# Kernel tuning notes

Hardware: AMD Instinct MI355X
Metric: run time of the kernel (lower is better)

## Reference

```python
import jax, jax.numpy as jnp
import numpy as np
from jax import lax

P = 4
PSIZE = P * P
ITERS = 3
EPS = 1e-8
LAMBDA = 1e-3  # inverse-temperature used by the EM routing sigmoid (yl-1993 style)
LN2PI_HALF = 0.5 * float(np.log(2.0 * np.pi))


def extract_patches(x, K, stride, pad):
    """x: (b,h,w,c) -> (b,oh,ow,K*K,c) sliding-window patches."""
    if pad:
        x = jnp.pad(x, ((0, 0), (pad, pad), (pad, pad), (0, 0)))
    b, h, w, c = x.shape
    oh = (h - K) // stride + 1
    ow = (w - K) // stride + 1
    slices = []
    for ki in range(K):
        for kj in range(K):
            slices.append(x[:, ki:ki + stride * (oh - 1) + 1:stride,
                             kj:kj + stride * (ow - 1) + 1:stride, :])
    return jnp.stack(slices, axis=3)  # (b,oh,ow,K*K,c)


def em_routing(v, a_in, beta_u, beta_a, iters=ITERS):
    """EM routing (Hinton et al. 2018).
    v: (n, Bin, Cout, PSIZE) votes, a_in: (n, Bin, 1) input activations.
    Returns mu: (n, Cout, PSIZE), a_out: (n, Cout).
    """
    n, Bin, Cout, psize = v.shape
    r = jnp.full((n, Bin, Cout), 1.0 / Cout, dtype=v.dtype)
    mu = None
    a_out = None
    for it in range(iters):
        # ---- M step ----
        r_w = r * a_in                                    # (n,Bin,Cout)
        r_sum = r_w.sum(axis=1, keepdims=True)            # (n,1,Cout)
        coeff = (r_w / (r_sum + EPS))[..., None]          # (n,Bin,Cout,1)
        mu = jnp.sum(coeff * v, axis=1, keepdims=True)    # (n,1,Cout,psize)
        sigma_sq = jnp.sum(coeff * (v - mu) ** 2, axis=1, keepdims=True) + EPS
        cost_h = (beta_u[None, None, :, None] + 0.5 * jnp.log(sigma_sq)) * r_sum[..., None]
        a_out = jax.nn.sigmoid(LAMBDA * (beta_a[None, None, :] - cost_h.sum(axis=3)))  # (n,1,Cout)
        # ---- E step ----
        if it < iters - 1:
            ln_p = -(v - mu) ** 2 / (2.0 * sigma_sq) - 0.5 * jnp.log(sigma_sq) - LN2PI_HALF
            ln_ap = ln_p.sum(axis=3) + jnp.log(EPS + a_out)  # (n,Bin,Cout)
            r = jax.nn.softmax(ln_ap, axis=2)
    return mu[:, 0], a_out[:, 0]


def depthwise_caps(pose, a, W, bu, ba, K, stride):
    """DepthWiseConvCaps: each capsule type routes its own KxK spatial patch to one
    output capsule of the same type. W: (K*K, B, P, P)."""
    b = pose.shape[0]
    Bc = a.shape[-1]
    pad = K // 2
    pp = extract_patches(pose, K, stride, pad)  # (b,oh,ow,KK,B*PSIZE)
    ap = extract_patches(a, K, stride, pad)     # (b,oh,ow,KK,B)
    oh, ow = pp.shape[1], pp.shape[2]
    pm = pp.reshape(b, oh, ow, K * K, Bc, P, P)
    v = jnp.einsum('bhwkcij,kcjl->bhwkcil', pm, W)            # (b,oh,ow,KK,B,P,P)
    v = v.transpose(0, 1, 2, 4, 3, 5, 6).reshape(b * oh * ow * Bc, K * K, 1, PSIZE)
    a_in = ap.transpose(0, 1, 2, 4, 3).reshape(b * oh * ow * Bc, K * K, 1)
    mu, a_out = em_routing(v, a_in, bu, ba)
    return mu.reshape(b, oh, ow, Bc * PSIZE), a_out.reshape(b, oh, ow, Bc)


def conv_caps_1x1(pose, a, W, bu, ba):
    """ConvCaps with K=1, stride=1: per-position routing Bin -> Cout. W: (Bin,Cout,P,P)."""
    b, h, w, _ = pose.shape
    Bc, Cc = W.shape[0], W.shape[1]
    pm = pose.reshape(b * h * w, Bc, P, P)
    v = jnp.einsum('nbij,bcjl->nbcil', pm, W).reshape(b * h * w, Bc, Cc, PSIZE)
    a_in = a.reshape(b * h * w, Bc)[..., None]
    mu, a_out = em_routing(v, a_in, bu, ba)
    return mu.reshape(b, h, w, Cc * PSIZE), a_out.reshape(b, h, w, Cc)


def class_caps(pose, a, W, bu, ba):
    """Class ConvCaps: w_shared across positions + coordinate addition. W: (D,E,P,P)."""
    b, h, w, _ = pose.shape
    D, E = W.shape[0], W.shape[1]
    pm = pose.reshape(b, h, w, D, P, P)
    v = jnp.einsum('bhwdij,dejl->bhwdeil', pm, W).reshape(b, h, w, D, E, PSIZE)
    # coordinate addition on the first two vote components
    coord = jnp.zeros((h, w, PSIZE), v.dtype)
    coord = coord.at[:, :, 0].add(jnp.arange(h, dtype=v.dtype)[:, None] / h)
    coord = coord.at[:, :, 1].add(jnp.arange(w, dtype=v.dtype)[None, :] / w)
    v = v + coord[None, :, :, None, None, :]
    v = v.reshape(b, h * w * D, E, PSIZE)
    a_in = a.reshape(b, h * w * D, 1)
    mu, a_out = em_routing(v, a_in, bu, ba)
    return mu, a_out  # (b,E,PSIZE), (b,E)


def _forward(x, conv1_w, conv1_b, prim_pose_w, prim_pose_b, prim_a_w, prim_a_b,
             dw1_w, dw1_bu, dw1_ba, cc1_w, cc1_bu, cc1_ba,
             dw2_w, dw2_bu, dw2_ba, cc2_w, cc2_bu, cc2_ba,
             cls_w, cls_bu, cls_ba):
    # conv stem: k5 s2 valid
    y = lax.conv_general_dilated(x, conv1_w, (2, 2), 'VALID',
                                 dimension_numbers=('NHWC', 'HWIO', 'NHWC'))
    y = jax.nn.relu(y + conv1_b)
    # primary caps: 1x1 convs for pose and activation
    pose = jnp.einsum('bhwc,cd->bhwd', y, prim_pose_w) + prim_pose_b   # (b,h,w,B*PSIZE)
    a = jax.nn.sigmoid(jnp.einsum('bhwc,cd->bhwd', y, prim_a_w) + prim_a_b)  # (b,h,w,B)
    pose, a = depthwise_caps(pose, a, dw1_w, dw1_bu, dw1_ba, K=7, stride=2)
    pose, a = conv_caps_1x1(pose, a, cc1_w, cc1_bu, cc1_ba)
    pose, a = depthwise_caps(pose, a, dw2_w, dw2_bu, dw2_ba, K=5, stride=2)
    pose, a = conv_caps_1x1(pose, a, cc2_w, cc2_bu, cc2_ba)
    pose_cls, a_cls = class_caps(pose, a, cls_w, cls_bu, cls_ba)
    return a_cls  # (b, E)


def setup_inputs() -> dict:
    key = jax.random.key(0)
    ks = jax.random.split(key, 10)
    f32 = jnp.float32
    d = {}
    d['x'] = jax.random.normal(ks[0], (32, 64, 64, 1), f32)
    d['conv1_w'] = jax.random.normal(ks[1], (5, 5, 1, 64), f32) * 0.1
    d['conv1_b'] = jnp.zeros((64,), f32)
    d['prim_pose_w'] = jax.random.normal(ks[2], (64, 128), f32) * 0.1
    d['prim_pose_b'] = jnp.zeros((128,), f32)
    d['prim_a_w'] = jax.random.normal(ks[3], (64, 8), f32) * 0.1
    d['prim_a_b'] = jnp.zeros((8,), f32)
    d['dw1_w'] = jax.random.normal(ks[4], (49, 8, 4, 4), f32) * 0.25
    d['dw1_bu'] = jnp.zeros((1,), f32)
    d['dw1_ba'] = jnp.zeros((1,), f32)
    d['cc1_w'] = jax.random.normal(ks[5], (8, 16, 4, 4), f32) * 0.25
    d['cc1_bu'] = jnp.zeros((16,), f32)
    d['cc1_ba'] = jnp.zeros((16,), f32)
    d['dw2_w'] = jax.random.normal(ks[6], (25, 16, 4, 4), f32) * 0.25
    d['dw2_bu'] = jnp.zeros((1,), f32)
    d['dw2_ba'] = jnp.zeros((1,), f32)
    d['cc2_w'] = jax.random.normal(ks[7], (16, 16, 4, 4), f32) * 0.25
    d['cc2_bu'] = jnp.zeros((16,), f32)
    d['cc2_ba'] = jnp.zeros((16,), f32)
    d['cls_w'] = jax.random.normal(ks[8], (16, 10, 4, 4), f32) * 0.25
    d['cls_bu'] = jnp.zeros((10,), f32)
    d['cls_ba'] = jnp.zeros((10,), f32)
    return d


def reference(x, conv1_w, conv1_b, prim_pose_w, prim_pose_b, prim_a_w, prim_a_b,
              dw1_w, dw1_bu, dw1_ba, cc1_w, cc1_bu, cc1_ba,
              dw2_w, dw2_bu, dw2_ba, cc2_w, cc2_bu, cc2_ba,
              cls_w, cls_bu, cls_ba):
    return _forward(x, conv1_w, conv1_b, prim_pose_w, prim_pose_b, prim_a_w, prim_a_b,
                    dw1_w, dw1_bu, dw1_ba, cc1_w, cc1_bu, cc1_ba,
                    dw2_w, dw2_bu, dw2_ba, cc2_w, cc2_bu, cc2_ba,
                    cls_w, cls_bu, cls_ba)
```

## Files before the change

### kernel.cpp

```cpp
#include <hip/hip_runtime.h>
#include <hip/hip_bf16.h>

#define EPS 1e-8f
#define LAMBDA 1e-3f
#define LN2PI_HALF 0.9189385332046727f

__device__ __forceinline__ float sigmoidf(float x) { return 1.f / (1.f + __expf(-x)); }

__global__ __launch_bounds__(256) void stem_primary_kernel(
    const float* __restrict__ x, const float* __restrict__ w,
    const float* __restrict__ bias,
    const float* __restrict__ wp, const float* __restrict__ bp,
    const float* __restrict__ wa, const float* __restrict__ ba,
    float* __restrict__ pose, float* __restrict__ a) {
  __shared__ float wp_s[64][128];
  __shared__ float wc_s[25][64];
  __shared__ float wa_s[64][8];
  __shared__ float bias_s[64];
  __shared__ float bp_s[128];
  __shared__ float ba_s[8];
  __shared__ float xs[5][23];
  __shared__ float ys[10][64];

  int t = threadIdx.x;
  int jt = blockIdx.x % 3;
  int oi = (blockIdx.x / 3) % 30;
  int b  = blockIdx.x / 90;
  int oj0 = jt * 10;

  for (int q = t; q < 8192; q += 256) ((float*)wp_s)[q] = wp[q];
  for (int q = t; q < 1600; q += 256) ((float*)wc_s)[q] = w[q];
  for (int q = t; q < 512;  q += 256) ((float*)wa_s)[q] = wa[q];
  if (t < 64) bias_s[t] = bias[t];
  if (t < 128) bp_s[t] = bp[t];
  if (t < 8) ba_s[t] = ba[t];
  for (int q = t; q < 115; q += 256) {
    int ki = q / 23, kj = q % 23;
    xs[ki][kj] = x[(b * 64 + 2 * oi + ki) * 64 + 2 * oj0 + kj];
  }
  __syncthreads();

#pragma unroll
  for (int rep = 0; rep < 3; ++rep) {
    int q = rep * 256 + t;
    if (q < 640) {
      int pos = q >> 6, ch = q & 63;
      float s = bias_s[ch];
#pragma unroll
      for (int ki = 0; ki < 5; ++ki)
#pragma unroll
        for (int kj = 0; kj < 5; ++kj)
          s += xs[ki][2 * pos + kj] * wc_s[ki * 5 + kj][ch];
      ys[pos][ch] = fmaxf(s, 0.f);
    }
  }
  __syncthreads();

  int w_ = t >> 7, d = t & 127;
  float acc[5];
#pragma unroll
  for (int j = 0; j < 5; ++j) acc[j] = bp_s[d];
  for (int c = 0; c < 64; ++c) {
    float wv = wp_s[c][d];
#pragma unroll
    for (int j = 0; j < 5; ++j) acc[j] += ys[w_ + 2 * j][c] * wv;
  }
  size_t rowbase = (size_t)(b * 30 + oi) * 30 + oj0;
#pragma unroll
  for (int j = 0; j < 5; ++j)
    pose[(rowbase + w_ + 2 * j) * 128 + d] = acc[j];

  if (t < 80) {
    int pos = t >> 3, jj = t & 7;
    float s = ba_s[jj];
#pragma unroll 8
    for (int c = 0; c < 64; ++c) s += ys[pos][c] * wa_s[c][jj];
    a[(rowbase + pos) * 8 + jj] = sigmoidf(s);
  }
}

template <int K, int BC, int HIN, int WIN, int HOUT, int WOUT, int OIG, int NG>
__global__ __launch_bounds__(256) void dw_caps_kernel(
    const float* __restrict__ pose_in, const float* __restrict__ a_in,
    const float* __restrict__ Wt,
    const float* __restrict__ bu_p, const float* __restrict__ ba_p,
    float* __restrict__ pose_out, float* __restrict__ a_out) {
  constexpr int PAD = K / 2;
  constexpr int RA = (2 * (OIG - 1) + K < HIN) ? (2 * (OIG - 1) + K) : HIN;
  __shared__ float tp[RA * WIN * 20];
  __shared__ float ta[RA * WIN];
  __shared__ float wt[K * K * 16];

  int t = threadIdx.x;
  int g = (NG > 1) ? (blockIdx.x % NG) : 0;
  int c = (blockIdx.x / NG) % BC;
  int b = blockIdx.x / (NG * BC);
  int oi_lo = g * OIG;
  int rlo = max(0, 2 * oi_lo - PAD);
  int rhi = min(HIN, 2 * (oi_lo + OIG - 1) - PAD + K);
  int nrows = rhi - rlo;

  for (int q = t; q < K * K * 16; q += 256) {
    int tap = q >> 4, lj = q & 15, l = lj >> 2, j = lj & 3;
    wt[tap * 16 + lj] = Wt[((size_t)tap * BC + c) * 16 + j * 4 + l];
  }
  for (int q = t; q < nrows * WIN; q += 256) {
    int row = q / WIN, col = q % WIN;
    ta[q] = a_in[((size_t)((b * HIN + rlo + row) * WIN + col)) * BC + c];
  }
  for (int q = t; q < nrows * WIN * 4; q += 256) {
    int quad = q & 3, pc = q >> 2;
    int row = pc / WIN, col = pc % WIN;
    const float4 src = *(const float4*)(pose_in +
        (((size_t)((b * HIN + rlo + row) * WIN + col)) * BC + c) * 16 + quad * 4);
    *(float4*)(tp + (row * WIN + col) * 20 + quad * 4) = src;
  }
  __syncthreads();

  for (int s = t; s < OIG * WOUT * 16; s += 256) {
    int p = s & 15, pr = s >> 4;
    int oj = pr % WOUT;
    int oi = oi_lo + pr / WOUT;
    int ip = p >> 2, l = p & 3;
    int ih0 = 2 * oi - PAD, iw0 = 2 * oj - PAD;
    float rsum = 0.f, acc = 0.f, acc2 = 0.f;
#pragma unroll
    for (int ki = 0; ki < K; ++ki) {
      int ih = ih0 + ki;
      if (ih < 0 || ih >= HIN) continue;
      int rbase = (ih - rlo) * WIN;
#pragma unroll
      for (int kj = 0; kj < K; ++kj) {
        int iw = iw0 + kj;
        if (iw < 0 || iw >= WIN) continue;
        float ak = ta[rbase + iw];
        const float4 pm = *(const float4*)(tp + (rbase + iw) * 20 + ip * 4);
        const float4 wr = *(const float4*)(wt + (ki * K + kj) * 16 + l * 4);
        float v = pm.x * wr.x + pm.y * wr.y + pm.z * wr.z + pm.w * wr.w;
        rsum += ak;
        float av = ak * v;
        acc += av;
        acc2 += av * v;
      }
    }
    float inv = 1.f / (rsum + EPS);
    float mu = acc * inv;
    float S = rsum * inv;
    float sg = acc2 * inv - mu * mu * (2.f - S);
    sg = fmaxf(sg, 0.f) + EPS;
    float hl = 0.5f * __logf(sg);
    float ls = hl;
    ls += __shfl_xor(ls, 1, 64);
    ls += __shfl_xor(ls, 2, 64);
    ls += __shfl_xor(ls, 4, 64);
    ls += __shfl_xor(ls, 8, 64);

    size_t obase = ((size_t)(b * HOUT + oi) * WOUT + oj) * BC + c;
    pose_out[obase * 16 + p] = mu;
    if (p == 0) {
      float cost = rsum * (16.f * bu_p[0] + ls);
      a_out[obase] = sigmoidf(LAMBDA * (ba_p[0] - cost));
    }
  }
}

template <int BIN>
__global__ __launch_bounds__(256) void cc_em_kernel(
    const float* __restrict__ pose_in, const float* __restrict__ a_arr,
    const float* __restrict__ Wt,
    const float* __restrict__ bu_p, const float* __restrict__ ba_p,
    float* __restrict__ pose_out, float* __restrict__ a_out) {
  constexpr int COUT = 16;
  __shared__ float pm_s[BIN * 16];
  __shared__ float ain_s[BIN];
  __shared__ float v_s[BIN][COUT * 16];
  __shared__ float rw_s[BIN][COUT];
  __shared__ float mu_s[COUT * 16];
  __shared__ float sg_s[COUT * 16];
  __shared__ float hl_s[COUT * 16];
  __shared__ float rsum_s[COUT];
  __shared__ float aout_s[COUT];
  __shared__ float lnap_s[BIN][COUT];

  int n = blockIdx.x, t = threadIdx.x;
  int c = t >> 4, p = t & 15;
  if (t < BIN * 16) pm_s[t] = pose_in[(size_t)n * BIN * 16 + t];
  if (t < BIN) ain_s[t] = a_arr[(size_t)n * BIN + t];
  __syncthreads();

  int ip = p >> 2, l = p & 3;
#pragma unroll
  for (int b = 0; b < BIN; ++b) {
    const float* wr = Wt + (b * COUT + c) * 16 + l;
    const float* pm = &pm_s[b * 16 + ip * 4];
    v_s[b][t] = pm[0] * wr[0] + pm[1] * wr[4] + pm[2] * wr[8] + pm[3] * wr[12];
  }
  if (t < BIN * COUT) rw_s[t / COUT][t % COUT] = (1.f / COUT) * ain_s[t / COUT];
  __syncthreads();

  for (int it = 0; it < 3; ++it) {
    if (t < COUT) {
      float s = 0.f;
#pragma unroll
      for (int b = 0; b < BIN; ++b) s += rw_s[b][t];
      rsum_s[t] = s;
    }
    __syncthreads();
    {
      float s = 0.f;
#pragma unroll
      for (int b = 0; b < BIN; ++b) s += rw_s[b][c] * v_s[b][t];
      float mu = s / (rsum_s[c] + EPS);
      mu_s[t] = mu;
      float s2 = 0.f;
#pragma unroll
      for (int b = 0; b < BIN; ++b) { float d = v_s[b][t] - mu; s2 += rw_s[b][c] * d * d; }
      float sg = s2 / (rsum_s[c] + EPS) + EPS;
      sg_s[t] = sg;
      hl_s[t] = 0.5f * __logf(sg);
    }
    __syncthreads();
    if (t < COUT) {
      float lsum = 0.f;
#pragma unroll
      for (int pp = 0; pp < 16; ++pp) lsum += hl_s[t * 16 + pp];
      float cost = rsum_s[t] * (16.f * bu_p[t] + lsum);
      aout_s[t] = sigmoidf(LAMBDA * (ba_p[t] - cost));
    }
    __syncthreads();
    if (it < 2) {
      if (t < BIN * COUT) {
        int b = t / COUT, cc = t % COUT;
        float s = __logf(EPS + aout_s[cc]) - 16.f * LN2PI_HALF;
#pragma unroll
        for (int pp = 0; pp < 16; ++pp) {
          float d = v_s[b][cc * 16 + pp] - mu_s[cc * 16 + pp];
          s += -d * d / (2.f * sg_s[cc * 16 + pp]) - hl_s[cc * 16 + pp];
        }
        lnap_s[b][cc] = s;
      }
      __syncthreads();
      if (t < BIN * COUT) {
        int b = t / COUT, cc = t % COUT;
        float m = -1e30f;
#pragma unroll
        for (int q = 0; q < COUT; ++q) m = fmaxf(m, lnap_s[b][q]);
        float Z = 0.f;
#pragma unroll
        for (int q = 0; q < COUT; ++q) Z += __expf(lnap_s[b][q] - m);
        rw_s[b][cc] = (__expf(lnap_s[b][cc] - m) / Z) * ain_s[b];
      }
      __syncthreads();
    }
  }
  pose_out[(size_t)n * COUT * 16 + t] = mu_s[t];
  if (t < COUT) a_out[(size_t)n * COUT + t] = aout_s[t];
}

__global__ __launch_bounds__(256) void cls_m_kernel(
    const float* __restrict__ pose5, const float* __restrict__ a5,
    const float* __restrict__ X, const float* __restrict__ W,
    const float* __restrict__ bu_p, const float* __restrict__ ba_p,
    float* __restrict__ mu_g, float* __restrict__ inv2_g,
    float* __restrict__ base_g, float* __restrict__ out,
    int first, int last) {
  int blk = blockIdx.x;
  int c = blk % 10, b = blk / 10;
  int t = threadIdx.x;
  int lane = t & 63, wv = t >> 6;
  const float* pg = pose5 + (size_t)b * 16384;
  __shared__ float w_s[16][16];
  {
    int d = t & 15, jj = t >> 4;
    w_s[jj][d] = W[(d * 10 + c) * 16 + jj];
  }
  __syncthreads();
  const int d = t & 15;
  float wf[16];
#pragma unroll
  for (int jj = 0; jj < 16; ++jj) wf[jj] = w_s[jj][d];

  float sA = 0.f, sV[16], sV2[16];
#pragma unroll
  for (int p = 0; p < 16; ++p) { sV[p] = 0.f; sV2[p] = 0.f; }
#pragma unroll
  for (int rep = 0; rep < 4; ++rep) {
    int bi = rep * 256 + t;
    int pos = bi >> 4;
    float rw = first ? 0.1f * a5[(size_t)b * 1024 + bi]
                     : X[(size_t)blk * 1024 + bi];
    float ci = (float)(pos >> 3) * 0.125f;
    float cj = (float)(pos & 7) * 0.125f;
    const float* pp = pg + pos * 256 + d * 16;
    float pmr[16];
#pragma unroll
    for (int q = 0; q < 16; ++q) pmr[q] = pp[q];
    sA += rw;
#pragma unroll
    for (int p = 0; p < 16; ++p) {
      int ip = p >> 2, l = p & 3;
      float v = pmr[ip * 4 + 0] * wf[0 * 4 + l] + pmr[ip * 4 + 1] * wf[1 * 4 + l]
              + pmr[ip * 4 + 2] * wf[2 * 4 + l] + pmr[ip * 4 + 3] * wf[3 * 4 + l];
      if (p == 0) v += ci;
      else if (p == 1) v += cj;
      float rv = rw * v;
      sV[p] += rv;
      sV2[p] += rv * v;
    }
  }
#pragma unroll
  for (int off = 1; off < 64; off <<= 1) {
    sA += __shfl_xor(sA, off, 64);
#pragma unroll
    for (int p = 0; p < 16; ++p) {
      sV[p]  += __shfl_xor(sV[p],  off, 64);
      sV2[p] += __shfl_xor(sV2[p], off, 64);
    }
  }
  __shared__ float red[4][36];
  if (lane == 0) {
    red[wv][0] = sA;
#pragma unroll
    for (int p = 0; p < 16; ++p) { red[wv][1 + p] = sV[p]; red[wv][17 + p] = sV2[p]; }
  }
  __syncthreads();
  if (t < 16) {
    int p = t;
    float sAf  = red[0][0] + red[1][0] + red[2][0] + red[3][0];
    float sVf  = red[0][1+p] + red[1][1+p] + red[2][1+p] + red[3][1+p];
    float sV2f = red[0][17+p] + red[1][17+p] + red[2][17+p] + red[3][17+p];
    float inv = 1.f / (sAf + EPS);
    float S = sAf * inv;
    float mu = sVf * inv;
    float sg = sV2f * inv - mu * mu * (2.f - S) + EPS;
    sg = fmaxf(sg, EPS);
    mu_g[blk * 16 + p] = mu;
    inv2_g[blk * 16 + p] = 0.5f / sg;
    float hl = 0.5f * __logf(sg);
    float lsum = hl;
    lsum += __shfl_xor(lsum, 1, 64);
    lsum += __shfl_xor(lsum, 2, 64);
    lsum += __shfl_xor(lsum, 4, 64);
    lsum += __shfl_xor(lsum, 8, 64);
    if (p == 0) {
      float cost = sAf * (16.f * bu_p[c] + lsum);
      float ao = sigmoidf(LAMBDA * (ba_p[c] - cost));
      base_g[blk] = __logf(EPS + ao) - lsum - 16.f * LN2PI_HALF;
      if (last) out[blk] = ao;
    }
  }
}

__global__ __launch_bounds__(512) void cls_e_kernel(
    const float* __restrict__ pose5, const float* __restrict__ a5,
    const float* __restrict__ W,
    const float* __restrict__ mu_g, const float* __restrict__ inv2_g,
    const float* __restrict__ base_g, float* __restrict__ X) {
  int b = blockIdx.x >> 1;
  int t = threadIdx.x;
  int bi = ((blockIdx.x & 1) << 9) + t;
  const float* pg = pose5 + (size_t)b * 16384;
  __shared__ float w2[10][16][16];
  __shared__ float mu_s[160];
  __shared__ float inv2_s[160];
  __shared__ float base_s[10];
  for (int q = t; q < 2560; q += 512) {
    int dd = q & 15, jj = (q >> 4) & 15, c = q >> 8;
    w2[c][jj][dd] = W[(dd * 10 + c) * 16 + jj];
  }
  if (t < 160) { mu_s[t] = mu_g[b * 160 + t]; inv2_s[t] = inv2_g[b * 160 + t]; }
  if (t >= 160 && t < 170) base_s[t - 160] = base_g[b * 10 + (t - 160)];
  __syncthreads();

  int pos = bi >> 4, d2 = bi & 15;
  float ci = (float)(pos >> 3) * 0.125f;
  float cj = (float)(pos & 7) * 0.125f;
  const float* pp = pg + pos * 256 + d2 * 16;
  float pmr[16];
#pragma unroll
  for (int q = 0; q < 16; ++q) pmr[q] = pp[q];
  float lnap[10];
#pragma unroll
  for (int c = 0; c < 10; ++c) {
    float wf[16];
#pragma unroll
    for (int jj = 0; jj < 16; ++jj) wf[jj] = w2[c][jj][d2];
    float s = base_s[c];
#pragma unroll
    for (int p = 0; p < 16; ++p) {
      int ip = p >> 2, l = p & 3;
      float v = pmr[ip * 4 + 0] * wf[0 * 4 + l] + pmr[ip * 4 + 1] * wf[1 * 4 + l]
              + pmr[ip * 4 + 2] * wf[2 * 4 + l] + pmr[ip * 4 + 3] * wf[3 * 4 + l];
      if (p == 0) v += ci;
      else if (p == 1) v += cj;
      float dd = v - mu_s[c * 16 + p];
      s -= dd * dd * inv2_s[c * 16 + p];
    }
    lnap[c] = s;
  }
  float m = -1e30f;
#pragma unroll
  for (int c = 0; c < 10; ++c) m = fmaxf(m, lnap[c]);
  float Z = 0.f;
  float ex[10];
#pragma unroll
  for (int c = 0; c < 10; ++c) { ex[c] = __expf(lnap[c] - m); Z += ex[c]; }
  float invZ = a5[(size_t)b * 1024 + bi] / Z;
#pragma unroll
  for (int c = 0; c < 10; ++c) X[((size_t)(b * 10 + c)) * 1024 + bi] = ex[c] * invZ;
}

extern "C" void kernel_launch(void* const* d_in, const int* in_sizes, int n_in,
                              void* d_out, int out_size, void* d_ws, size_t ws_size,
                              hipStream_t stream) {
  const float* x       = (const float*)d_in[0];
  const float* conv1_w = (const float*)d_in[1];
  const float* conv1_b = (const float*)d_in[2];
  const float* pp_w    = (const float*)d_in[3];
  const float* pp_b    = (const float*)d_in[4];
  const float* pa_w    = (const float*)d_in[5];
  const float* pa_b    = (const float*)d_in[6];
  const float* dw1_w   = (const float*)d_in[7];
  const float* dw1_bu  = (const float*)d_in[8];
  const float* dw1_ba  = (const float*)d_in[9];
  const float* cc1_w   = (const float*)d_in[10];
  const float* cc1_bu  = (const float*)d_in[11];
  const float* cc1_ba  = (const float*)d_in[12];
  const float* dw2_w   = (const float*)d_in[13];
  const float* dw2_bu  = (const float*)d_in[14];
  const float* dw2_ba  = (const float*)d_in[15];
  const float* cc2_w   = (const float*)d_in[16];
  const float* cc2_bu  = (const float*)d_in[17];
  const float* cc2_ba  = (const float*)d_in[18];
  const float* cls_w   = (const float*)d_in[19];
  const float* cls_bu  = (const float*)d_in[20];
  const float* cls_ba  = (const float*)d_in[21];
  float* out = (float*)d_out;

  float* ws = (float*)d_ws;
  float* pose1 = ws;
  float* a1    = ws + 3686400;
  float* pose2 = ws + 3916800;
  float* a2    = ws + 4838400;
  float* pose3 = ws;
  float* a3    = ws + 1843200;
  float* pose4 = ws + 1958400;
  float* a4    = ws + 2482688;
  float* pose5 = ws + 2515456;
  float* a5    = ws + 3039744;
  float* Xbuf  = ws + 3072512;
  float* mu_g  = ws + 3400192;
  float* inv2_g= ws + 3405312;
  float* base_g= ws + 3410432;

  stem_primary_kernel<<<2880, 256, 0, stream>>>(x, conv1_w, conv1_b,
                                                pp_w, pp_b, pa_w, pa_b, pose1, a1);
  dw_caps_kernel<7, 8, 30, 30, 15, 15, 5, 3><<<768, 256, 0, stream>>>(
      pose1, a1, dw1_w, dw1_bu, dw1_ba, pose2, a2);
  cc_em_kernel<8><<<7200, 256, 0, stream>>>(pose2, a2, cc1_w, cc1_bu, cc1_ba, pose3, a3);
  dw_caps_kernel<5, 16, 15, 15, 8, 8, 8, 1><<<512, 256, 0, stream>>>(
      pose3, a3, dw2_w, dw2_bu, dw2_ba, pose4, a4);
  cc_em_kernel<16><<<2048, 256, 0, stream>>>(pose4, a4, cc2_w, cc2_bu, cc2_ba, pose5, a5);
  cls_m_kernel<<<320, 256, 0, stream>>>(pose5, a5, Xbuf, cls_w, cls_bu, cls_ba,
                                        mu_g, inv2_g, base_g, out, 1, 0);
  cls_e_kernel<<<64, 512, 0, stream>>>(pose5, a5, cls_w, mu_g, inv2_g, base_g, Xbuf);
  cls_m_kernel<<<320, 256, 0, stream>>>(pose5, a5, Xbuf, cls_w, cls_bu, cls_ba,
                                        mu_g, inv2_g, base_g, out, 0, 0);
  cls_e_kernel<<<64, 512, 0, stream>>>(pose5, a5, cls_w, mu_g, inv2_g, base_g, Xbuf);
  cls_m_kernel<<<320, 256, 0, stream>>>(pose5, a5, Xbuf, cls_w, cls_bu, cls_ba,
                                        mu_g, inv2_g, base_g, out, 0, 1);
}
```

Baseline: 286.2 us.

## Keep votes in registers and use one-pass variance with shuffle reductions in cc EM kernel

Rewrites the convolutional-capsule EM routing kernel so each thread holds its votes in registers and no longer stores them to shared memory. The weighted mean and variance are computed in one pass from sums of r, r·v and r·v², with the cost term and E-step log-likelihood reduced through 16-lane shuffles, which removes several shared arrays and block barriers. Weights are staged in shared memory first. The one-pass variance formula is less numerically robust than the original two-pass form, so it is clamped at EPS.

```diff
diff --git a/kernel.cpp b/kernel.cpp
--- a/kernel.cpp
+++ b/kernel.cpp
@@ -171,90 +171,82 @@
     const float* __restrict__ bu_p, const float* __restrict__ ba_p,
     float* __restrict__ pose_out, float* __restrict__ a_out) {
   constexpr int COUT = 16;
+  __shared__ float w_s[BIN * COUT * 16];
   __shared__ float pm_s[BIN * 16];
   __shared__ float ain_s[BIN];
-  __shared__ float v_s[BIN][COUT * 16];
   __shared__ float rw_s[BIN][COUT];
-  __shared__ float mu_s[COUT * 16];
-  __shared__ float sg_s[COUT * 16];
-  __shared__ float hl_s[COUT * 16];
-  __shared__ float rsum_s[COUT];
-  __shared__ float aout_s[COUT];
-  __shared__ float lnap_s[BIN][COUT];
+  __shared__ float lnap_s[BIN][17];
 
   int n = blockIdx.x, t = threadIdx.x;
   int c = t >> 4, p = t & 15;
+  int ip = p >> 2, l = p & 3;
+
+  for (int q = t; q < BIN * COUT * 16; q += 256) w_s[q] = Wt[q];
   if (t < BIN * 16) pm_s[t] = pose_in[(size_t)n * BIN * 16 + t];
   if (t < BIN) ain_s[t] = a_arr[(size_t)n * BIN + t];
-  __syncthreads();
-
-  int ip = p >> 2, l = p & 3;
+  if (t < BIN * COUT) rw_s[t >> 4][t & 15] = (1.f / COUT) * a_arr[(size_t)n * BIN + (t >> 4)];
+  float bu = bu_p[c], ba = ba_p[c];
+  __syncthreads();
+
+  float v[BIN];
 #pragma unroll
   for (int b = 0; b < BIN; ++b) {
-    const float* wr = Wt + (b * COUT + c) * 16 + l;
-    const float* pm = &pm_s[b * 16 + ip * 4];
-    v_s[b][t] = pm[0] * wr[0] + pm[1] * wr[4] + pm[2] * wr[8] + pm[3] * wr[12];
-  }
-  if (t < BIN * COUT) rw_s[t / COUT][t % COUT] = (1.f / COUT) * ain_s[t / COUT];
-  __syncthreads();
-
+    const float* wr = w_s + (b * COUT + c) * 16 + l;
+    const float* pm = pm_s + b * 16 + ip * 4;
+    v[b] = pm[0] * wr[0] + pm[1] * wr[4] + pm[2] * wr[8] + pm[3] * wr[12];
+  }
+
+  float mu = 0.f, ao = 0.f;
   for (int it = 0; it < 3; ++it) {
-    if (t < COUT) {
-      float s = 0.f;
-#pragma unroll
-      for (int b = 0; b < BIN; ++b) s += rw_s[b][t];
-      rsum_s[t] = s;
-    }
-    __syncthreads();
-    {
-      float s = 0.f;
-#pragma unroll
-      for (int b = 0; b < BIN; ++b) s += rw_s[b][c] * v_s[b][t];
-      float mu = s / (rsum_s[c] + EPS);
-      mu_s[t] = mu;
-      float s2 = 0.f;
-#pragma unroll
-      for (int b = 0; b < BIN; ++b) { float d = v_s[b][t] - mu; s2 += rw_s[b][c] * d * d; }
-      float sg = s2 / (rsum_s[c] + EPS) + EPS;
-      sg_s[t] = sg;
-      hl_s[t] = 0.5f * __logf(sg);
-    }
-    __syncthreads();
-    if (t < COUT) {
-      float lsum = 0.f;
-#pragma unroll
-      for (int pp = 0; pp < 16; ++pp) lsum += hl_s[t * 16 + pp];
-      float cost = rsum_s[t] * (16.f * bu_p[t] + lsum);
-      aout_s[t] = sigmoidf(LAMBDA * (ba_p[t] - cost));
-    }
-    __syncthreads();
+    float sA = 0.f, sV = 0.f, sV2 = 0.f;
+#pragma unroll
+    for (int b = 0; b < BIN; ++b) {
+      float rw = rw_s[b][c];
+      sA += rw;
+      float rv = rw * v[b];
+      sV += rv;
+      sV2 += rv * v[b];
+    }
+    float inv = 1.f / (sA + EPS);
+    mu = sV * inv;
+    float S = sA * inv;
+    float sg = sV2 * inv - mu * mu * (2.f - S) + EPS;
+    sg = fmaxf(sg, EPS);
+    float hl = 0.5f * __logf(sg);
+    float inv2 = 0.5f / sg;
+    float hlsum = hl;
+    hlsum += __shfl_xor(hlsum, 1, 16);
+    hlsum += __shfl_xor(hlsum, 2, 16);
+    hlsum += __shfl_xor(hlsum, 4, 16);
+    hlsum += __shfl_xor(hlsum, 8, 16);
+    float cost = sA * (16.f * bu + hlsum);
+    ao = sigmoidf(LAMBDA * (ba - cost));
     if (it < 2) {
+      float red[BIN];
+#pragma unroll
+      for (int b = 0; b < BIN; ++b) { float d = v[b] - mu; red[b] = d * d * inv2; }
+#pragma unroll
+      for (int m = 1; m < 16; m <<= 1)
+#pragma unroll
+        for (int b = 0; b < BIN; ++b) red[b] += __shfl_xor(red[b], m, 16);
+      if (p < BIN)
+        lnap_s[p][c] = __logf(EPS + ao) - hlsum - 16.f * LN2PI_HALF - red[p];
+      __syncthreads();
       if (t < BIN * COUT) {
-        int b = t / COUT, cc = t % COUT;
-        float s = __logf(EPS + aout_s[cc]) - 16.f * LN2PI_HALF;
-#pragma unroll
-        for (int pp = 0; pp < 16; ++pp) {
-          float d = v_s[b][cc * 16 + pp] - mu_s[cc * 16 + pp];
-          s += -d * d / (2.f * sg_s[cc * 16 + pp]) - hl_s[cc * 16 + pp];
-        }
-        lnap_s[b][cc] = s;
+        int b = t >> 4, cc = t & 15;
+        float mx = -1e30f;
+#pragma unroll
+        for (int q = 0; q < COUT; ++q) mx = fmaxf(mx, lnap_s[b][q]);
+        float Z = 0.f;
+#pragma unroll
+        for (int q = 0; q < COUT; ++q) Z += __expf(lnap_s[b][q] - mx);
+        rw_s[b][cc] = (__expf(lnap_s[b][cc] - mx) / Z) * ain_s[b];
       }
       __syncthreads();
-      if (t < BIN * COUT) {
-        int b = t / COUT, cc = t % COUT;
-        float m = -1e30f;
-#pragma unroll
-        for (int q = 0; q < COUT; ++q) m = fmaxf(m, lnap_s[b][q]);
-        float Z = 0.f;
-#pragma unroll
-        for (int q = 0; q < COUT; ++q) Z += __expf(lnap_s[b][q] - m);
-        rw_s[b][cc] = (__expf(lnap_s[b][cc] - m) / Z) * ain_s[b];
-      }
-      __syncthreads();
-    }
-  }
-  pose_out[(size_t)n * COUT * 16 + t] = mu_s[t];
-  if (t < COUT) a_out[(size_t)n * COUT + t] = aout_s[t];
+    }
+  }
+  pose_out[(size_t)n * COUT * 16 + t] = mu;
+  if (p == 0) a_out[(size_t)n * COUT + c] = ao;
 }
 
 __global__ __launch_bounds__(256) void cls_m_kernel(
```

Measured after the change: 284.6 us. No clear change (-0.6%).
